# Performance work log

Measured on AMD Instinct MI355X. Metric: run time of the kernel, lower is better.

The kernel has to match this reference:

```python
import jax, jax.numpy as jnp
import numpy as np


def setup_inputs() -> dict:
    key = jax.random.key(0)
    ks = jax.random.split(key, 5)
    B, C, H, W = 8, 256, 64, 64
    Ck = C // 8  # 32, reduced channel dim
    return {
        "x": jax.random.normal(ks[0], (B, C, H, W), dtype=jnp.float32),
        "wf": jax.random.normal(ks[1], (Ck, C), dtype=jnp.float32) * 0.05,
        "wg": jax.random.normal(ks[2], (Ck, C), dtype=jnp.float32) * 0.05,
        "wh": jax.random.normal(ks[3], (Ck, C), dtype=jnp.float32) * 0.05,
        "wv": jax.random.normal(ks[4], (C, Ck), dtype=jnp.float32) * 0.05,
        "gamma": jnp.zeros((1,), dtype=jnp.float32),
    }


def reference(x, wf, wg, wh, wv, gamma):
    B, C, H, W = x.shape
    N = H * W
    xf = x.reshape(B, C, N)  # flatten spatial tokens
    # 1x1 convs == channel matmuls
    f = jnp.einsum('oc,bcn->bon', wf, xf)  # [B, Ck, N]
    g = jnp.einsum('oc,bcn->bon', wg, xf)  # [B, Ck, N]
    h = jnp.einsum('oc,bcn->bon', wh, xf)  # [B, Ck, N]
    # s = f^T @ g -> [B, N, N]; softmax over last axis (dim 2 in torch)
    s = jnp.einsum('bcn,bcm->bnm', f, g)
    beta = jax.nn.softmax(s, axis=2)
    # v = h @ beta  (note: beta NOT transposed, faithful to original)
    v = jnp.einsum('bcn,bnm->bcm', h, beta)  # [B, Ck, N]
    o = jnp.einsum('oc,bcm->bom', wv, v).reshape(B, C, H, W)
    return gamma * o + x
```

## Files before the change

### kernel.cpp

```cpp
#include <hip/hip_runtime.h>
#include <hip/hip_bf16.h>

#define BB 8
#define CC 256
#define CK 32
#define NN 4096

typedef short bf16x8 __attribute__((ext_vector_type(8)));
typedef float f32x4 __attribute__((ext_vector_type(4)));

#define MFMA(a, b, c) __builtin_amdgcn_mfma_f32_16x16x32_bf16((a), (b), (c), 0, 0, 0)

#define GLOAD16(gsrc, ldst) __builtin_amdgcn_global_load_lds( \
    (const __attribute__((address_space(1))) void*)(gsrc), \
    (__attribute__((address_space(3))) void*)(ldst), 16, 0, 0)

#define OBASE(b) ((size_t)(b) * 1048576)
#define OFF_F  0
#define OFF_G  65536
#define OFF_HT 131072
#define OFF_V0 200704
#define OFF_WB 786432
#define VSTRIDE 131072

#define SHIFT 24.0f

static __device__ __forceinline__ unsigned pack_trunc(float lo, float hi) {
  unsigned ulo = __builtin_bit_cast(unsigned, lo);
  unsigned uhi = __builtin_bit_cast(unsigned, hi);
  return (uhi & 0xFFFF0000u) | (ulo >> 16);
}
static __device__ __forceinline__ unsigned pack_rne(float lo, float hi) {
  unsigned ulo = __builtin_bit_cast(unsigned, lo);
  unsigned uhi = __builtin_bit_cast(unsigned, hi);
  ulo += 0x7FFFu + ((ulo >> 16) & 1u);
  uhi += 0x7FFFu + ((uhi >> 16) & 1u);
  return (uhi & 0xFFFF0000u) | (ulo >> 16);
}
static __device__ __forceinline__ unsigned short rne16(float v) {
  unsigned u = __builtin_bit_cast(unsigned, v);
  u += 0x7FFFu + ((u >> 16) & 1u);
  return (unsigned short)(u >> 16);
}

__global__ __launch_bounds__(256) void wcvt_kernel(
    const float* __restrict__ wf, const float* __restrict__ wg,
    const float* __restrict__ wh, float* __restrict__ sc)
{
  int w = blockIdx.x;
  int tid = threadIdx.x;
  const float* src = (w == 0) ? wf : ((w == 1) ? wg : wh);
  unsigned short* wb = (unsigned short*)(sc + OFF_WB) + w * 8192;
  for (int e = tid; e < 8192; e += 256) wb[e] = rne16(src[e]);
}

__global__ __launch_bounds__(256) void proj_kernel(
    const float* __restrict__ x, float* __restrict__ sc)
{
  __shared__ float t[64][69];
  __shared__ unsigned short tb[64][264];

  int tid = threadIdx.x, blk = blockIdx.x;
  int b = blk >> 6, n0 = (blk & 63) << 6;

  #pragma unroll 1
  for (int ct = 0; ct < 4; ++ct) {
    int c0 = ct << 6;
    const float* xb = x + ((size_t)b * CC + c0) * NN + n0;
    int ci0 = tid >> 4, j = (tid & 15) << 2;
    #pragma unroll
    for (int p = 0; p < 4; ++p) {
      int ci = p * 16 + ci0;
      float4 v = *(const float4*)&xb[(size_t)ci * NN + j];
      t[ci][j] = v.x; t[ci][j + 1] = v.y; t[ci][j + 2] = v.z; t[ci][j + 3] = v.w;
    }
    __syncthreads();
    int ni = tid >> 2, cq = (tid & 3) << 4;
    #pragma unroll
    for (int e = 0; e < 16; ++e)
      tb[ni][c0 + cq + e] = rne16(t[cq + e][ni]);
    __syncthreads();
  }

  int w = tid >> 6, lane = tid & 63, q = lane >> 4, c = lane & 15;
  int nb = n0 + (w << 4);
  const char* wB = (const char*)(sc + OFF_WB);
  const unsigned short* tbrow = &tb[(w << 4) + c][0];

  const f32x4 z4 = {0.f, 0.f, 0.f, 0.f};
  f32x4 fa0 = z4, fa1 = z4, ga0 = z4, ga1 = z4, ha0 = z4, ha1 = z4;

  #pragma unroll
  for (int kc = 0; kc < 8; ++kc) {
    int koe = kc * 32 + q * 8;
    int ko = kc * 64 + q * 16;
    bf16x8 xa = *(const bf16x8*)(tbrow + koe);
    bf16x8 w0 = *(const bf16x8*)(wB + (size_t)c * 512 + ko);
    bf16x8 w1 = *(const bf16x8*)(wB + (size_t)(16 + c) * 512 + ko);
    bf16x8 w2 = *(const bf16x8*)(wB + 16384 + (size_t)c * 512 + ko);
    bf16x8 w3 = *(const bf16x8*)(wB + 16384 + (size_t)(16 + c) * 512 + ko);
    bf16x8 w4 = *(const bf16x8*)(wB + 32768 + (size_t)c * 512 + ko);
    bf16x8 w5 = *(const bf16x8*)(wB + 32768 + (size_t)(16 + c) * 512 + ko);
    fa0 = MFMA(xa, w0, fa0);  fa1 = MFMA(xa, w1, fa1);
    ga0 = MFMA(xa, w2, ga0);  ga1 = MFMA(xa, w3, ga1);
    ha0 = MFMA(w4, xa, ha0);  ha1 = MFMA(w5, xa, ha1);
  }

  unsigned short* fD = (unsigned short*)(sc + OBASE(b) + OFF_F);
  unsigned short* gD = (unsigned short*)(sc + OBASE(b) + OFF_G);
  unsigned short* hD = (unsigned short*)(sc + OBASE(b) + OFF_HT);
  #pragma unroll
  for (int r = 0; r < 4; ++r) {
    int n = nb + q * 4 + r;
    fD[(size_t)n * 32 + c]      = rne16(fa0[r]);
    fD[(size_t)n * 32 + 16 + c] = rne16(fa1[r]);
    gD[(size_t)n * 32 + c]      = rne16(ga0[r]);
    gD[(size_t)n * 32 + 16 + c] = rne16(ga1[r]);
    hD[(size_t)(q * 4 + r) * NN + nb + c]        = rne16(ha0[r]);
    hD[(size_t)(16 + q * 4 + r) * NN + nb + c]   = rne16(ha1[r]);
  }
}

__global__ __launch_bounds__(256) void passb_kernel(float* __restrict__ sc)
{
  __shared__ float Zsh[2][16][4];
  __shared__ float Rsh[32];
  int tid = threadIdx.x, blk = blockIdx.x;
  int b = blk >> 7, nb0 = (blk & 127) << 5;
  int w = tid >> 6, lane = tid & 63, q = lane >> 4, c = lane & 15;

  const char* fb = (const char*)(sc + OBASE(b) + OFF_F);
  const char* gb = (const char*)(sc + OBASE(b) + OFF_G);

  bf16x8 fa0 = *(const bf16x8*)(fb + (size_t)(nb0 + c) * 64 + q * 16);
  bf16x8 fa1 = *(const bf16x8*)(fb + (size_t)(nb0 + 16 + c) * 64 + q * 16);
  const f32x4 z4 = {0.f, 0.f, 0.f, 0.f};
  float za[2][4] = {{0.f,0.f,0.f,0.f},{0.f,0.f,0.f,0.f}};

  int mt0 = w << 10;
  bf16x8 g0 = *(const bf16x8*)(gb + (size_t)(mt0 + 0  + c) * 64 + q * 16);
  bf16x8 g1 = *(const bf16x8*)(gb + (size_t)(mt0 + 16 + c) * 64 + q * 16);
  bf16x8 g2 = *(const bf16x8*)(gb + (size_t)(mt0 + 32 + c) * 64 + q * 16);
  bf16x8 g3 = *(const bf16x8*)(gb + (size_t)(mt0 + 48 + c) * 64 + q * 16);

  for (int mt = mt0; mt < mt0 + 1024; mt += 64) {
    int mtn = (mt + 64 < mt0 + 1024) ? mt + 64 : mt0;
    bf16x8 n0 = *(const bf16x8*)(gb + (size_t)(mtn + 0  + c) * 64 + q * 16);
    bf16x8 n1 = *(const bf16x8*)(gb + (size_t)(mtn + 16 + c) * 64 + q * 16);
    bf16x8 n2 = *(const bf16x8*)(gb + (size_t)(mtn + 32 + c) * 64 + q * 16);
    bf16x8 n3 = *(const bf16x8*)(gb + (size_t)(mtn + 48 + c) * 64 + q * 16);
    f32x4 s;
    #define BSTEP(gk) \
      s = MFMA(fa0, gk, z4); \
      za[0][0] += __expf(s[0] - SHIFT); za[0][1] += __expf(s[1] - SHIFT); \
      za[0][2] += __expf(s[2] - SHIFT); za[0][3] += __expf(s[3] - SHIFT); \
      s = MFMA(fa1, gk, z4); \
      za[1][0] += __expf(s[0] - SHIFT); za[1][1] += __expf(s[1] - SHIFT); \
      za[1][2] += __expf(s[2] - SHIFT); za[1][3] += __expf(s[3] - SHIFT);
    BSTEP(g0) BSTEP(g1) BSTEP(g2) BSTEP(g3)
    #undef BSTEP
    g0 = n0; g1 = n1; g2 = n2; g3 = n3;
  }
  #pragma unroll
  for (int d = 1; d < 16; d <<= 1) {
    #pragma unroll
    for (int i = 0; i < 2; ++i)
      #pragma unroll
      for (int r = 0; r < 4; ++r) za[i][r] += __shfl_xor(za[i][r], d);
  }
  if (c == 0) {
    #pragma unroll
    for (int i = 0; i < 2; ++i)
      #pragma unroll
      for (int r = 0; r < 4; ++r) Zsh[i][q * 4 + r][w] = za[i][r];
  }
  __syncthreads();
  if (tid < 32) {
    int ns2 = tid >> 4, row = tid & 15;
    float Z = Zsh[ns2][row][0] + Zsh[ns2][row][1]
            + Zsh[ns2][row][2] + Zsh[ns2][row][3];
    Rsh[ns2 * 16 + row] = 1.0f / Z;
  }
  __syncthreads();
  {
    int cidx = tid >> 3, jj = (tid & 7) << 2;
    unsigned short* hp = (unsigned short*)(sc + OBASE(b) + OFF_HT)
                       + (size_t)cidx * NN + nb0 + jj;
    uint2 hv = *(const uint2*)hp;
    float h0 = __builtin_bit_cast(float, hv.x << 16)          * Rsh[jj + 0];
    float h1 = __builtin_bit_cast(float, hv.x & 0xFFFF0000u)  * Rsh[jj + 1];
    float h2 = __builtin_bit_cast(float, hv.y << 16)          * Rsh[jj + 2];
    float h3 = __builtin_bit_cast(float, hv.y & 0xFFFF0000u)  * Rsh[jj + 3];
    uint2 ov;
    ov.x = pack_rne(h0, h1);
    ov.y = pack_rne(h2, h3);
    *(uint2*)hp = ov;
  }
}

__global__ __launch_bounds__(256, 4) void passc_kernel(float* __restrict__ sc)
{
  __shared__ unsigned Pt[128 * 32 + 1024];
  __shared__ unsigned fsh[2][1024];
  __shared__ unsigned hsh[2][1024];

  int tid = threadIdx.x, blk = blockIdx.x;
  int b = blk >> 7, rest = blk & 127;
  int ns = rest & 3, mblk = rest >> 2;
  int m0 = mblk << 7;
  int nbase = ns << 10;
  int w = tid >> 6, lane = tid & 63, q = lane >> 4, c = lane & 15;
  int hc = tid >> 3, hslot = (tid & 7) ^ (hc & 7);

  const char* fb = (const char*)(sc + OBASE(b) + OFF_F);
  const char* gb = (const char*)(sc + OBASE(b) + OFF_G);
  const char* hb = (const char*)(sc + OBASE(b) + OFF_HT);

  bf16x8 gB0 = *(const bf16x8*)(gb + (size_t)(m0 + w * 16 + c) * 64 + q * 16);
  bf16x8 gB1 = *(const bf16x8*)(gb + (size_t)(m0 + 64 + w * 16 + c) * 64 + q * 16);

  GLOAD16(fb + (size_t)nbase * 64 + tid * 16, (char*)&fsh[0][0] + tid * 16);
  GLOAD16(hb + (size_t)hc * 8192 + (size_t)nbase * 2 + hslot * 16,
          (char*)&hsh[0][0] + tid * 16);
  __syncthreads();

  const f32x4 z4 = {0.f, 0.f, 0.f, 0.f};
  f32x4 v00 = z4, v01 = z4, v10 = z4, v11 = z4;

  unsigned sw = (unsigned)(c & 7) << 4;
  char* Pt0 = (char*)Pt + (size_t)(w * 16 + c) * 128;
  char* Pt1 = (char*)Pt + (size_t)(64 + w * 16 + c) * 128;

  int buf = 0;
  for (int nt = 0; nt < 1024; nt += 64) {
    if (nt + 64 < 1024) {
      GLOAD16(fb + (size_t)(nbase + nt + 64) * 64 + tid * 16,
              (char*)&fsh[buf ^ 1][0] + tid * 16);
      GLOAD16(hb + (size_t)hc * 8192 + (size_t)(nbase + nt + 64) * 2 + hslot * 16,
              (char*)&hsh[buf ^ 1][0] + tid * 16);
    }
    const char* fS = (const char*)&fsh[buf][0];
    const char* hS = (const char*)&hsh[buf][0];

    bf16x8 f0 = *(const bf16x8*)(fS + (0 * 16 + c) * 64 + q * 16);
    bf16x8 f1 = *(const bf16x8*)(fS + (1 * 16 + c) * 64 + q * 16);
    bf16x8 f2 = *(const bf16x8*)(fS + (2 * 16 + c) * 64 + q * 16);
    bf16x8 f3 = *(const bf16x8*)(fS + (3 * 16 + c) * 64 + q * 16);
    f32x4 sA0 = MFMA(f0, gB0, z4), sB0 = MFMA(f0, gB1, z4);
    f32x4 sA1 = MFMA(f1, gB0, z4), sB1 = MFMA(f1, gB1, z4);
    f32x4 sA2 = MFMA(f2, gB0, z4), sB2 = MFMA(f2, gB1, z4);
    f32x4 sA3 = MFMA(f3, gB0, z4), sB3 = MFMA(f3, gB1, z4);

    #pragma unroll
    for (int sub = 0; sub < 4; ++sub) {
      f32x4 sA = (sub == 0) ? sA0 : (sub == 1) ? sA1 : (sub == 2) ? sA2 : sA3;
      f32x4 sB = (sub == 0) ? sB0 : (sub == 1) ? sB1 : (sub == 2) ? sB2 : sB3;
      uint2 pkA, pkB;
      pkA.x = pack_trunc(__expf(sA[0] - SHIFT), __expf(sA[1] - SHIFT));
      pkA.y = pack_trunc(__expf(sA[2] - SHIFT), __expf(sA[3] - SHIFT));
      pkB.x = pack_trunc(__expf(sB[0] - SHIFT), __expf(sB[1] - SHIFT));
      pkB.y = pack_trunc(__expf(sB[2] - SHIFT), __expf(sB[3] - SHIFT));
      unsigned off = ((unsigned)(sub * 32 + q * 8)) ^ sw;
      *(uint2*)(Pt0 + off) = pkA;
      *(uint2*)(Pt1 + off) = pkB;
    }

    #pragma unroll
    for (int ks = 0; ks < 2; ++ks) {
      unsigned off = ((unsigned)(ks * 64 + q * 16)) ^ sw;
      bf16x8 pb0 = *(const bf16x8*)(Pt0 + off);
      bf16x8 pb1 = *(const bf16x8*)(Pt1 + off);
      bf16x8 h0 = *(const bf16x8*)(hS + c * 128 + off);
      bf16x8 h1 = *(const bf16x8*)(hS + (16 + c) * 128 + off);
      v00 = MFMA(h0, pb0, v00);
      v10 = MFMA(h1, pb0, v10);
      v01 = MFMA(h0, pb1, v01);
      v11 = MFMA(h1, pb1, v11);
    }
    __syncthreads();
    buf ^= 1;
  }

  float* V = sc + OBASE(b) + OFF_V0 + (size_t)ns * VSTRIDE;
  {
    int mA = m0 + w * 16 + c, mB = m0 + 64 + w * 16 + c;
    size_t bA = (size_t)(mA & 31) * 4096 + (size_t)(mA >> 5) * 32;
    size_t bB = (size_t)(mB & 31) * 4096 + (size_t)(mB >> 5) * 32;
    *(f32x4*)&V[bA + q * 4]      = v00;
    *(f32x4*)&V[bA + 16 + q * 4] = v10;
    *(f32x4*)&V[bB + q * 4]      = v01;
    *(f32x4*)&V[bB + 16 + q * 4] = v11;
  }
}

__global__ __launch_bounds__(256) void epi_kernel(
    float* out, const float* __restrict__ x,
    const float* __restrict__ wv, const float* __restrict__ gamma)
{
  __shared__ float vt[256][36];
  int tid = threadIdx.x, blk = blockIdx.x;
  int b = blk >> 7;
  int m0 = (blk & 127) << 5;
  int w = tid >> 6, lane = tid & 63, q = lane >> 4, c = lane & 15;
  int co0 = w << 6;

  const float* V0 = out + OBASE(b) + OFF_V0;

  bf16x8 Bf[2];
  #pragma unroll
  for (int mt = 0; mt < 2; ++mt) {
    int ml = mt * 16 + c;
    size_t base = (size_t)ml * 4096 + (size_t)(m0 >> 5) * 32 + q * 8;
    float4 a0 = {0,0,0,0}, a1 = {0,0,0,0};
    #pragma unroll
    for (int i = 0; i < 4; ++i) {
      const float* Vi = V0 + (size_t)i * VSTRIDE;
      float4 p0 = *(const float4*)&Vi[base];
      float4 p1 = *(const float4*)&Vi[base + 4];
      a0.x += p0.x; a0.y += p0.y; a0.z += p0.z; a0.w += p0.w;
      a1.x += p1.x; a1.y += p1.y; a1.z += p1.z; a1.w += p1.w;
    }
    unsigned u0 = pack_rne(a0.x, a0.y);
    unsigned u1 = pack_rne(a0.z, a0.w);
    unsigned u2 = pack_rne(a1.x, a1.y);
    unsigned u3 = pack_rne(a1.z, a1.w);
    Bf[mt] = __builtin_bit_cast(bf16x8, make_uint4(u0, u1, u2, u3));
  }
  bf16x8 Af[4];
  #pragma unroll
  for (int ci = 0; ci < 4; ++ci) {
    const float* wr = wv + (size_t)(co0 + ci * 16 + c) * 32 + q * 8;
    float4 a0 = *(const float4*)wr;
    float4 a1 = *(const float4*)(wr + 4);
    unsigned u0 = pack_rne(a0.x, a0.y);
    unsigned u1 = pack_rne(a0.z, a0.w);
    unsigned u2 = pack_rne(a1.x, a1.y);
    unsigned u3 = pack_rne(a1.z, a1.w);
    Af[ci] = __builtin_bit_cast(bf16x8, make_uint4(u0, u1, u2, u3));
  }

  const f32x4 z4 = {0.f, 0.f, 0.f, 0.f};
  #pragma unroll
  for (int ci = 0; ci < 4; ++ci) {
    #pragma unroll
    for (int mt = 0; mt < 2; ++mt) {
      f32x4 acc = MFMA(Af[ci], Bf[mt], z4);
      #pragma unroll
      for (int r = 0; r < 4; ++r)
        vt[co0 + ci * 16 + q * 4 + r][mt * 16 + c] = acc[r];
    }
  }
  __syncthreads();

  const float g0 = gamma[0];
  int rsub = lane >> 3, col = (lane & 7) << 2;
  #pragma unroll
  for (int p = 0; p < 8; ++p) {
    int row = (w << 6) + (p << 3) + rsub;
    f32x4 v = *(const f32x4*)&vt[row][col];
    size_t idx = ((size_t)b * CC + row) * NN + m0 + col;
    float4 xv = *(const float4*)&x[idx];
    float4 o;
    o.x = g0 * v[0] + xv.x;
    o.y = g0 * v[1] + xv.y;
    o.z = g0 * v[2] + xv.z;
    o.w = g0 * v[3] + xv.w;
    *(float4*)&out[idx] = o;
  }
}

extern "C" void kernel_launch(void* const* d_in, const int* in_sizes, int n_in,
                              void* d_out, int out_size, void* d_ws, size_t ws_size,
                              hipStream_t stream) {
  const float* x     = (const float*)d_in[0];
  const float* wf    = (const float*)d_in[1];
  const float* wg    = (const float*)d_in[2];
  const float* wh    = (const float*)d_in[3];
  const float* wv    = (const float*)d_in[4];
  const float* gamma = (const float*)d_in[5];
  float* out = (float*)d_out;

  wcvt_kernel <<<3,    256, 0, stream>>>(wf, wg, wh, out);
  proj_kernel <<<512,  256, 0, stream>>>(x, out);
  passb_kernel<<<1024, 256, 0, stream>>>(out);
  passc_kernel<<<1024, 256, 0, stream>>>(out);
  epi_kernel  <<<1024, 256, 0, stream>>>(out, x, wv, gamma);
}
```

Baseline: 107.6 us.

## Load f and h tiles directly into registers, drop LDS staging and barriers

The pass-C kernel no longer stages f and h tiles in LDS through async global-to-LDS loads with double buffering. Each wave now reads its f fragments and h operands straight from global memory into registers, prefetching the next f tile in software. This removes the per-iteration __syncthreads and the LDS traffic for those operands, and occupancy is raised to 8 blocks. In exchange, the four waves of a block fetch the same data redundantly through the cache. Register pressure also rises under the tighter occupancy bound, which may cause spills.

Result: slower. 151.0 us (+40.4%).

```diff
diff --git a/kernel.cpp b/kernel.cpp
--- a/kernel.cpp
+++ b/kernel.cpp
@@ -10,10 +10,6 @@
 typedef float f32x4 __attribute__((ext_vector_type(4)));
 
 #define MFMA(a, b, c) __builtin_amdgcn_mfma_f32_16x16x32_bf16((a), (b), (c), 0, 0, 0)
-
-#define GLOAD16(gsrc, ldst) __builtin_amdgcn_global_load_lds( \
-    (const __attribute__((address_space(1))) void*)(gsrc), \
-    (__attribute__((address_space(3))) void*)(ldst), 16, 0, 0)
 
 #define OBASE(b) ((size_t)(b) * 1048576)
 #define OFF_F  0
@@ -198,11 +194,9 @@
   }
 }
 
-__global__ __launch_bounds__(256, 4) void passc_kernel(float* __restrict__ sc)
-{
-  __shared__ unsigned Pt[128 * 32 + 1024];
-  __shared__ unsigned fsh[2][1024];
-  __shared__ unsigned hsh[2][1024];
+__global__ __launch_bounds__(256, 8) void passc_kernel(float* __restrict__ sc)
+{
+  __shared__ unsigned Pt[128 * 32];
 
   int tid = threadIdx.x, blk = blockIdx.x;
   int b = blk >> 7, rest = blk & 127;
@@ -210,7 +204,6 @@
   int m0 = mblk << 7;
   int nbase = ns << 10;
   int w = tid >> 6, lane = tid & 63, q = lane >> 4, c = lane & 15;
-  int hc = tid >> 3, hslot = (tid & 7) ^ (hc & 7);
 
   const char* fb = (const char*)(sc + OBASE(b) + OFF_F);
   const char* gb = (const char*)(sc + OBASE(b) + OFF_G);
@@ -219,11 +212,6 @@
   bf16x8 gB0 = *(const bf16x8*)(gb + (size_t)(m0 + w * 16 + c) * 64 + q * 16);
   bf16x8 gB1 = *(const bf16x8*)(gb + (size_t)(m0 + 64 + w * 16 + c) * 64 + q * 16);
 
-  GLOAD16(fb + (size_t)nbase * 64 + tid * 16, (char*)&fsh[0][0] + tid * 16);
-  GLOAD16(hb + (size_t)hc * 8192 + (size_t)nbase * 2 + hslot * 16,
-          (char*)&hsh[0][0] + tid * 16);
-  __syncthreads();
-
   const f32x4 z4 = {0.f, 0.f, 0.f, 0.f};
   f32x4 v00 = z4, v01 = z4, v10 = z4, v11 = z4;
 
@@ -231,25 +219,27 @@
   char* Pt0 = (char*)Pt + (size_t)(w * 16 + c) * 128;
   char* Pt1 = (char*)Pt + (size_t)(64 + w * 16 + c) * 128;
 
-  int buf = 0;
+  bf16x8 fc0 = *(const bf16x8*)(fb + (size_t)(nbase + 0  + c) * 64 + q * 16);
+  bf16x8 fc1 = *(const bf16x8*)(fb + (size_t)(nbase + 16 + c) * 64 + q * 16);
+  bf16x8 fc2 = *(const bf16x8*)(fb + (size_t)(nbase + 32 + c) * 64 + q * 16);
+  bf16x8 fc3 = *(const bf16x8*)(fb + (size_t)(nbase + 48 + c) * 64 + q * 16);
+
   for (int nt = 0; nt < 1024; nt += 64) {
-    if (nt + 64 < 1024) {
-      GLOAD16(fb + (size_t)(nbase + nt + 64) * 64 + tid * 16,
-              (char*)&fsh[buf ^ 1][0] + tid * 16);
-      GLOAD16(hb + (size_t)hc * 8192 + (size_t)(nbase + nt + 64) * 2 + hslot * 16,
-              (char*)&hsh[buf ^ 1][0] + tid * 16);
-    }
-    const char* fS = (const char*)&fsh[buf][0];
-    const char* hS = (const char*)&hsh[buf][0];
-
-    bf16x8 f0 = *(const bf16x8*)(fS + (0 * 16 + c) * 64 + q * 16);
-    bf16x8 f1 = *(const bf16x8*)(fS + (1 * 16 + c) * 64 + q * 16);
-    bf16x8 f2 = *(const bf16x8*)(fS + (2 * 16 + c) * 64 + q * 16);
-    bf16x8 f3 = *(const bf16x8*)(fS + (3 * 16 + c) * 64 + q * 16);
-    f32x4 sA0 = MFMA(f0, gB0, z4), sB0 = MFMA(f0, gB1, z4);
-    f32x4 sA1 = MFMA(f1, gB0, z4), sB1 = MFMA(f1, gB1, z4);
-    f32x4 sA2 = MFMA(f2, gB0, z4), sB2 = MFMA(f2, gB1, z4);
-    f32x4 sA3 = MFMA(f3, gB0, z4), sB3 = MFMA(f3, gB1, z4);
+    bf16x8 ha00 = *(const bf16x8*)(hb + (size_t)c * 8192        + (size_t)(nbase + nt + q * 8) * 2);
+    bf16x8 ha01 = *(const bf16x8*)(hb + (size_t)c * 8192        + (size_t)(nbase + nt + 32 + q * 8) * 2);
+    bf16x8 ha10 = *(const bf16x8*)(hb + (size_t)(16 + c) * 8192 + (size_t)(nbase + nt + q * 8) * 2);
+    bf16x8 ha11 = *(const bf16x8*)(hb + (size_t)(16 + c) * 8192 + (size_t)(nbase + nt + 32 + q * 8) * 2);
+
+    f32x4 sA0 = MFMA(fc0, gB0, z4), sB0 = MFMA(fc0, gB1, z4);
+    f32x4 sA1 = MFMA(fc1, gB0, z4), sB1 = MFMA(fc1, gB1, z4);
+    f32x4 sA2 = MFMA(fc2, gB0, z4), sB2 = MFMA(fc2, gB1, z4);
+    f32x4 sA3 = MFMA(fc3, gB0, z4), sB3 = MFMA(fc3, gB1, z4);
+
+    int ntn = (nt + 64 < 1024) ? nt + 64 : 0;
+    bf16x8 fn0 = *(const bf16x8*)(fb + (size_t)(nbase + ntn + 0  + c) * 64 + q * 16);
+    bf16x8 fn1 = *(const bf16x8*)(fb + (size_t)(nbase + ntn + 16 + c) * 64 + q * 16);
+    bf16x8 fn2 = *(const bf16x8*)(fb + (size_t)(nbase + ntn + 32 + c) * 64 + q * 16);
+    bf16x8 fn3 = *(const bf16x8*)(fb + (size_t)(nbase + ntn + 48 + c) * 64 + q * 16);
 
     #pragma unroll
     for (int sub = 0; sub < 4; ++sub) {
@@ -270,15 +260,14 @@
       unsigned off = ((unsigned)(ks * 64 + q * 16)) ^ sw;
       bf16x8 pb0 = *(const bf16x8*)(Pt0 + off);
       bf16x8 pb1 = *(const bf16x8*)(Pt1 + off);
-      bf16x8 h0 = *(const bf16x8*)(hS + c * 128 + off);
-      bf16x8 h1 = *(const bf16x8*)(hS + (16 + c) * 128 + off);
+      bf16x8 h0 = ks ? ha01 : ha00;
+      bf16x8 h1 = ks ? ha11 : ha10;
       v00 = MFMA(h0, pb0, v00);
       v10 = MFMA(h1, pb0, v10);
       v01 = MFMA(h0, pb1, v01);
       v11 = MFMA(h1, pb1, v11);
     }
-    __syncthreads();
-    buf ^= 1;
+    fc0 = fn0; fc1 = fn1; fc2 = fn2; fc3 = fn3;
   }
 
   float* V = sc + OBASE(b) + OFF_V0 + (size_t)ns * VSTRIDE;
```
